# Optimization experiments

Measured on AMD Instinct MI355X. Metric: run time of the kernel, lower is better.

Reference implementation:

```python
import jax, jax.numpy as jnp
import numpy as np

NENTITY = 200000
NRELATION = 500
HIDDEN = 256
GAMMA = 12.0
EPS = 2.0
EMB_RANGE = (GAMMA + EPS) / HIDDEN


def setup_inputs() -> dict:
    key = jax.random.key(0)
    ks = jax.random.split(key, 8)
    B, NEG = 256, 1024
    head = jax.random.randint(ks[0], (B, 1), 0, NENTITY)
    tail = jax.random.randint(ks[1], (B, NEG), 0, NENTITY)
    relation = jax.random.randint(ks[2], (B,), 0, NRELATION)
    entity_emb = jax.random.uniform(ks[3], (NENTITY, HIDDEN), jnp.float32, -EMB_RANGE, EMB_RANGE)
    relation_emb = jax.random.uniform(ks[4], (NRELATION, 2 * HIDDEN), jnp.float32, -EMB_RANGE, EMB_RANGE)
    lim = 1.0 / np.sqrt(2 * HIDDEN)
    W_fc = jax.random.uniform(ks[5], (HIDDEN, 2 * HIDDEN), jnp.float32, -lim, lim)
    b_fc = jax.random.uniform(ks[6], (HIDDEN,), jnp.float32, -lim, lim)
    return {"head": head, "tail": tail, "relation": relation,
            "entity_emb": entity_emb, "relation_emb": relation_emb,
            "W_fc": W_fc, "b_fc": b_fc}


def _l2_normalize(x):
    # F.normalize(x, p=2, dim=-1): x / max(||x||_2, 1e-12)
    n = jnp.sqrt(jnp.sum(x * x, axis=-1, keepdims=True))
    return x / jnp.maximum(n, 1e-12)


def reference(head, tail, relation, entity_emb, relation_emb, W_fc, b_fc):
    # gather embeddings
    h = entity_emb[head]                      # [B, 1,   d]
    t = entity_emb[tail]                      # [B, NEG, d]
    r = relation_emb[relation][:, None, :]    # [B, 1, 2d]
    re_head, re_tail = jnp.split(r, 2, axis=-1)   # each [B, 1, d]
    # broadcast relation halves to match head/tail sample counts, then concat
    re_h = jnp.broadcast_to(re_head, h.shape)
    re_t = jnp.broadcast_to(re_tail, t.shape)
    h_cat = jnp.concatenate([h, re_h], axis=-1)   # [B, 1,   2d]
    t_cat = jnp.concatenate([t, re_t], axis=-1)   # [B, NEG, 2d]
    # shared small FC (torch Linear: x @ W^T + b)
    h_fc = jnp.einsum('bnk,dk->bnd', h_cat, W_fc) + b_fc
    t_fc = jnp.einsum('bnk,dk->bnd', t_cat, W_fc) + b_fc
    h_n = _l2_normalize(h_fc)
    t_n = _l2_normalize(t_fc)
    diff = h_n - t_n                              # [B, NEG, d]
    score = GAMMA - jnp.sum(jnp.abs(diff), axis=2)  # [B, NEG]
    return score
```

## Files before the change

kernel.cpp:

```cpp
#include <hip/hip_runtime.h>
#include <math.h>

#define NENTITY 200000
#define HIDDEN 256
#define NEG 1024
#define NBATCH 256
#define GAMMA_F 12.0f
#define BM 32
#define NTILES 8
#define NBLK 1024
#define NT_P 8
#define CHUNK 128

typedef short v8s __attribute__((ext_vector_type(8)));
typedef float v4f __attribute__((ext_vector_type(4)));
typedef unsigned int u32;

#define LDS_BARRIER() asm volatile("s_waitcnt lgkmcnt(0)\n\ts_barrier" ::: "memory")

__device__ __forceinline__ short f2bf(float x) {
    u32 u = __float_as_uint(x);
    u = (u + 0x7fffu + ((u >> 16) & 1u)) >> 16;
    return (short)u;
}

__device__ __forceinline__ u32 rhu(float f) { return __float_as_uint(f) + 0x8000u; }
__device__ __forceinline__ v8s pack8(const float4& x0, const float4& x1) {
    int4 fr;
    fr.x = __builtin_amdgcn_perm(rhu(x0.y), rhu(x0.x), 0x07060302u);
    fr.y = __builtin_amdgcn_perm(rhu(x0.w), rhu(x0.z), 0x07060302u);
    fr.z = __builtin_amdgcn_perm(rhu(x1.y), rhu(x1.x), 0x07060302u);
    fr.w = __builtin_amdgcn_perm(rhu(x1.w), rhu(x1.z), 0x07060302u);
    return __builtin_bit_cast(v8s, fr);
}
__device__ __forceinline__ uint2 pack4(const v4f& a) {
    uint2 pk;
    pk.x = __builtin_amdgcn_perm(rhu(a[1]), rhu(a[0]), 0x07060302u);
    pk.y = __builtin_amdgcn_perm(rhu(a[3]), rhu(a[2]), 0x07060302u);
    return pk;
}

__global__ __launch_bounds__(256) void prep_kernel(
    const int* __restrict__ head, const int* __restrict__ relation,
    const float* __restrict__ entity_emb, const float* __restrict__ relation_emb,
    const float* __restrict__ W_fc, const float* __restrict__ b_fc,
    short* __restrict__ W1bf, float* __restrict__ h_n, float* __restrict__ rel_part)
{
    const int b = blockIdx.x;
    const int t = threadIdx.x;

    W1bf[b * HIDDEN + t] = f2bf(W_fc[(size_t)b * 2 * HIDDEN + t]);

    __shared__ float xh[2 * HIDDEN];
    __shared__ float xt[HIDDEN];
    __shared__ float red[256];

    const int hidx = head[b];
    const int r = relation[b];
    xh[t]          = entity_emb[(size_t)hidx * HIDDEN + t];
    xh[HIDDEN + t] = relation_emb[(size_t)r * 2 * HIDDEN + t];
    xt[t]          = relation_emb[(size_t)r * 2 * HIDDEN + HIDDEN + t];
    __syncthreads();

    const float4* wrow = reinterpret_cast<const float4*>(W_fc + (size_t)t * 2 * HIDDEN);
    float hf = b_fc[t];
    float rp = b_fc[t];
    #pragma unroll 4
    for (int kk = 0; kk < HIDDEN / 4; ++kk) {
        float4 w = wrow[kk];
        hf += xh[4*kk+0]*w.x + xh[4*kk+1]*w.y + xh[4*kk+2]*w.z + xh[4*kk+3]*w.w;
    }
    #pragma unroll 4
    for (int kk = 0; kk < HIDDEN / 4; ++kk) {
        float4 w = wrow[HIDDEN/4 + kk];
        hf += xh[HIDDEN+4*kk+0]*w.x + xh[HIDDEN+4*kk+1]*w.y + xh[HIDDEN+4*kk+2]*w.z + xh[HIDDEN+4*kk+3]*w.w;
        rp += xt[4*kk+0]*w.x + xt[4*kk+1]*w.y + xt[4*kk+2]*w.z + xt[4*kk+3]*w.w;
    }
    rel_part[b * HIDDEN + t] = rp;

    red[t] = hf * hf;
    __syncthreads();
    for (int s = 128; s > 0; s >>= 1) {
        if (t < s) red[t] += red[t + s];
        __syncthreads();
    }
    const float norm = sqrtf(red[0]);
    h_n[b * HIDDEN + t] = hf / fmaxf(norm, 1e-12f);
}

__global__ __launch_bounds__(512, 4) void proj_kernel(
    const float* __restrict__ entity_emb, const short* __restrict__ W1bf,
    short* __restrict__ P)
{
    __shared__ __align__(16) short Abf[2][BM * HIDDEN];

    const int t = threadIdx.x;
    const int w = t >> 6;
    const int l = t & 63;
    const int c = t & 15;
    const int g = (t >> 4) & 3;
    const int E0 = blockIdx.x * (NT_P * BM);

    v8s Wf[2][8];
    #pragma unroll
    for (int f2 = 0; f2 < 2; ++f2) {
        const short* bsrc = W1bf + (size_t)(w * 32 + f2 * 16 + c) * HIDDEN + g * 8;
        #pragma unroll
        for (int kt = 0; kt < 8; ++kt)
            Wf[f2][kt] = *reinterpret_cast<const v8s*>(bsrc + kt * 32);
    }
    #pragma unroll
    for (int f2 = 0; f2 < 2; ++f2)
        #pragma unroll
        for (int kt = 0; kt < 8; ++kt)
            asm volatile("" : "+v"(Wf[f2][kt]));

    v4f st[4];
    auto issue = [&](int j) {
        #pragma unroll
        for (int i = 0; i < 4; ++i) {
            int row = E0 + j * BM + w * 4 + i;
            row = row < NENTITY ? row : NENTITY - 1;
            st[i] = *reinterpret_cast<const v4f*>(
                entity_emb + (size_t)row * HIDDEN + (l << 2));
        }
        __builtin_amdgcn_sched_barrier(0);
    };
    auto commit = [&](int buf) {
        char* base = reinterpret_cast<char*>(&Abf[buf][0]);
        #pragma unroll
        for (int i = 0; i < 4; ++i) {
            const int r = w * 4 + i;
            uint2 pk = pack4(st[i]);
            *reinterpret_cast<uint2*>(base + r * 512
                + (((l >> 1) ^ (r & 7)) << 4) + ((l & 1) << 3)) = pk;
        }
    };

    issue(0);
    commit(0);
    LDS_BARRIER();

    #pragma unroll 1
    for (int j = 0; j < NT_P; ++j) {
        const int cur = j & 1;
        if (j + 1 < NT_P) issue(j + 1);

        v4f acc[2][2];
        #pragma unroll
        for (int et = 0; et < 2; ++et)
            #pragma unroll
            for (int f2 = 0; f2 < 2; ++f2)
                acc[et][f2] = v4f{0.f, 0.f, 0.f, 0.f};

        const char* base = reinterpret_cast<const char*>(&Abf[cur][0]);
        const int swz = c & 7;

        #pragma unroll
        for (int kt = 0; kt < 8; ++kt) {
            const int u = ((kt * 4 + g) ^ swz) << 4;
            v8s e0 = *reinterpret_cast<const v8s*>(base + (c)      * 512 + u);
            v8s e1 = *reinterpret_cast<const v8s*>(base + (16 + c) * 512 + u);
            #pragma unroll
            for (int f2 = 0; f2 < 2; ++f2) {
                acc[0][f2] = __builtin_amdgcn_mfma_f32_16x16x32_bf16(Wf[f2][kt], e0, acc[0][f2], 0, 0, 0);
                acc[1][f2] = __builtin_amdgcn_mfma_f32_16x16x32_bf16(Wf[f2][kt], e1, acc[1][f2], 0, 0, 0);
            }
        }

        if (j + 1 < NT_P) commit(cur ^ 1);

        #pragma unroll
        for (int et = 0; et < 2; ++et) {
            const int e = E0 + j * BM + et * 16 + c;
            if (e < NENTITY) {
                short* dst = P + (size_t)e * HIDDEN + w * 32 + g * 4;
                #pragma unroll
                for (int f2 = 0; f2 < 2; ++f2)
                    *reinterpret_cast<uint2*>(dst + f2 * 16) = pack4(acc[et][f2]);
            }
        }

        LDS_BARRIER();
    }
}

__global__ __launch_bounds__(256) void score2_kernel(
    const int* __restrict__ tail, const short* __restrict__ P,
    const float* __restrict__ h_n, const float* __restrict__ rel_part,
    float* __restrict__ out)
{
    const int t = threadIdx.x;
    const int w = t >> 6;
    const int l = t & 63;
    const int b = blockIdx.x >> 3;
    const int chunk = blockIdx.x & 7;
    const int base = b * NEG + chunk * CHUNK;

    __shared__ int tl[CHUNK];
    if (t < CHUNK) tl[t] = tail[base + t];

    const float4 hh = *reinterpret_cast<const float4*>(h_n + b * HIDDEN + 4 * l);
    const float4 rp = *reinterpret_cast<const float4*>(rel_part + b * HIDDEN + 4 * l);
    __syncthreads();

    uint2 st2[8];
    #pragma unroll
    for (int i = 0; i < 8; ++i)
        st2[i] = *(reinterpret_cast<const uint2*>(P + (size_t)tl[w * 32 + i] * HIDDEN) + l);

    #pragma unroll
    for (int p = 0; p < 32; ++p) {
        uint2 v = st2[p & 7];
        if (p + 8 < 32)
            st2[p & 7] = *(reinterpret_cast<const uint2*>(
                P + (size_t)tl[w * 32 + p + 8] * HIDDEN) + l);

        float t0 = __uint_as_float(v.x << 16)          + rp.x;
        float t1 = __uint_as_float(v.x & 0xffff0000u)  + rp.y;
        float t2 = __uint_as_float(v.y << 16)          + rp.z;
        float t3 = __uint_as_float(v.y & 0xffff0000u)  + rp.w;

        float ssq = t0 * t0 + t1 * t1 + t2 * t2 + t3 * t3;
        #pragma unroll
        for (int mask = 1; mask < 64; mask <<= 1) ssq += __shfl_xor(ssq, mask);
        const float rn = 1.f / fmaxf(sqrtf(ssq), 1e-12f);

        float l1 = fabsf(hh.x - t0 * rn) + fabsf(hh.y - t1 * rn)
                 + fabsf(hh.z - t2 * rn) + fabsf(hh.w - t3 * rn);
        #pragma unroll
        for (int mask = 1; mask < 64; mask <<= 1) l1 += __shfl_xor(l1, mask);

        if (l == 0) out[base + w * 32 + p] = GAMMA_F - l1;
    }
}

__global__ __launch_bounds__(256, 2) void score_kernel(
    const int* __restrict__ tail, const float* __restrict__ entity_emb,
    const short* __restrict__ W1bf, const float* __restrict__ h_n,
    const float* __restrict__ rel_part, float* __restrict__ out)
{
    __shared__ __align__(16) float Asf[2][BM * HIDDEN];
    __shared__ int tails[NTILES * BM];
    __shared__ float ssq_lds[4][BM];
    __shared__ float l1_lds[4][BM];

    const int t = threadIdx.x;
    const int w = t >> 6;
    const int l = t & 63;
    const int c = t & 15;
    const int g = (t >> 4) & 3;
    const int b = blockIdx.x >> 2;

    tails[t] = tail[blockIdx.x * (NTILES * BM) + t];

    float rlv[4], hnv[4];
    #pragma unroll
    for (int ntl = 0; ntl < 4; ++ntl) {
        const int n = 64 * w + ntl * 16 + c;
        rlv[ntl] = rel_part[b * HIDDEN + n];
        hnv[ntl] = h_n[b * HIDDEN + n];
    }

    v8s Bf[4][8];
    #pragma unroll
    for (int ntl = 0; ntl < 4; ++ntl) {
        const short* bsrc = W1bf + (size_t)(64 * w + ntl * 16 + c) * HIDDEN + g * 8;
        #pragma unroll
        for (int kt = 0; kt < 8; ++kt)
            Bf[ntl][kt] = *reinterpret_cast<const v8s*>(bsrc + kt * 32);
    }

    __syncthreads();

    v4f st[8];
    auto issue = [&](int j) {
        #pragma unroll
        for (int i = 0; i < 8; ++i) {
            const int r = w * 8 + i;
            const float* src = entity_emb + (size_t)tails[j * BM + r] * HIDDEN + (l << 2);
            st[i] = *reinterpret_cast<const v4f*>(src);
        }
        __builtin_amdgcn_sched_barrier(0);
    };
    auto commit = [&](int buf) {
        #pragma unroll
        for (int i = 0; i < 8; ++i) {
            const int r = w * 8 + i;
            *reinterpret_cast<v4f*>(&Asf[buf][r * HIDDEN + ((l ^ (r & 7)) << 2)]) = st[i];
        }
    };

    issue(0);
    commit(0);
    LDS_BARRIER();

    #pragma unroll 1
    for (int j = 0; j < NTILES; ++j) {
        const int cur = j & 1;
        if (j + 1 < NTILES) issue(j + 1);

        v4f acc[2][4];
        #pragma unroll
        for (int mt = 0; mt < 2; ++mt)
            #pragma unroll
            for (int ntl = 0; ntl < 4; ++ntl)
                acc[mt][ntl] = v4f{0.f, 0.f, 0.f, 0.f};

        const float* a0base = &Asf[cur][c * HIDDEN];
        const float* a1base = &Asf[cur][(16 + c) * HIDDEN];
        const int swz = c & 7;

        #pragma unroll
        for (int kt = 0; kt < 8; ++kt) {
            const int u0 = kt * 8 + g * 2;
            float4 x0 = *reinterpret_cast<const float4*>(a0base + (((u0    ) ^ swz) << 2));
            float4 x1 = *reinterpret_cast<const float4*>(a0base + (((u0 + 1) ^ swz) << 2));
            float4 y0 = *reinterpret_cast<const float4*>(a1base + (((u0    ) ^ swz) << 2));
            float4 y1 = *reinterpret_cast<const float4*>(a1base + (((u0 + 1) ^ swz) << 2));
            v8s a0 = pack8(x0, x1);
            v8s a1 = pack8(y0, y1);
            #pragma unroll
            for (int ntl = 0; ntl < 4; ++ntl) {
                acc[0][ntl] = __builtin_amdgcn_mfma_f32_16x16x32_bf16(a0, Bf[ntl][kt], acc[0][ntl], 0, 0, 0);
                acc[1][ntl] = __builtin_amdgcn_mfma_f32_16x16x32_bf16(a1, Bf[ntl][kt], acc[1][ntl], 0, 0, 0);
            }
        }

        #pragma unroll
        for (int mt = 0; mt < 2; ++mt) {
            float ssq[4] = {0.f, 0.f, 0.f, 0.f};
            #pragma unroll
            for (int ntl = 0; ntl < 4; ++ntl) {
                #pragma unroll
                for (int r = 0; r < 4; ++r) {
                    float tf = acc[mt][ntl][r] + rlv[ntl];
                    acc[mt][ntl][r] = tf;
                    ssq[r] += tf * tf;
                }
            }
            #pragma unroll
            for (int mask = 1; mask < 16; mask <<= 1) {
                #pragma unroll
                for (int r = 0; r < 4; ++r) ssq[r] += __shfl_xor(ssq[r], mask);
            }
            if (c == 0) {
                #pragma unroll
                for (int r = 0; r < 4; ++r) ssq_lds[w][mt * 16 + g * 4 + r] = ssq[r];
            }
        }
        LDS_BARRIER();

        #pragma unroll
        for (int mt = 0; mt < 2; ++mt) {
            float rn[4], s1[4] = {0.f, 0.f, 0.f, 0.f};
            #pragma unroll
            for (int r = 0; r < 4; ++r) {
                const int m = mt * 16 + g * 4 + r;
                float tot = ssq_lds[0][m] + ssq_lds[1][m] + ssq_lds[2][m] + ssq_lds[3][m];
                rn[r] = 1.f / fmaxf(sqrtf(tot), 1e-12f);
            }
            #pragma unroll
            for (int ntl = 0; ntl < 4; ++ntl) {
                #pragma unroll
                for (int r = 0; r < 4; ++r)
                    s1[r] += fabsf(hnv[ntl] - acc[mt][ntl][r] * rn[r]);
            }
            #pragma unroll
            for (int mask = 1; mask < 16; mask <<= 1) {
                #pragma unroll
                for (int r = 0; r < 4; ++r) s1[r] += __shfl_xor(s1[r], mask);
            }
            if (c == 0) {
                #pragma unroll
                for (int r = 0; r < 4; ++r) l1_lds[w][mt * 16 + g * 4 + r] = s1[r];
            }
        }

        if (j + 1 < NTILES) commit(cur ^ 1);
        LDS_BARRIER();

        if (t < BM) {
            out[blockIdx.x * (NTILES * BM) + j * BM + t] = GAMMA_F -
                (l1_lds[0][t] + l1_lds[1][t] + l1_lds[2][t] + l1_lds[3][t]);
        }
    }
}

extern "C" void kernel_launch(void* const* d_in, const int* in_sizes, int n_in,
                              void* d_out, int out_size, void* d_ws, size_t ws_size,
                              hipStream_t stream)
{
    const int*   head         = (const int*)d_in[0];
    const int*   tail         = (const int*)d_in[1];
    const int*   relation     = (const int*)d_in[2];
    const float* entity_emb   = (const float*)d_in[3];
    const float* relation_emb = (const float*)d_in[4];
    const float* W_fc         = (const float*)d_in[5];
    const float* b_fc         = (const float*)d_in[6];
    float* out = (float*)d_out;

    short* W1bf     = (short*)d_ws;
    float* h_n      = (float*)((char*)d_ws + 131072);
    float* rel_part = (float*)((char*)d_ws + 131072 + 262144);

    prep_kernel<<<NBATCH, 256, 0, stream>>>(head, relation, entity_emb, relation_emb,
                                            W_fc, b_fc, W1bf, h_n, rel_part);

    const size_t P_OFF   = 1ull << 20;
    const size_t P_BYTES = (size_t)NENTITY * HIDDEN * sizeof(short);
    if (ws_size >= P_OFF + P_BYTES) {
        short* P = (short*)((char*)d_ws + P_OFF);
        const int grid = (NENTITY + NT_P * BM - 1) / (NT_P * BM);
        proj_kernel<<<grid, 512, 0, stream>>>(entity_emb, W1bf, P);
        score2_kernel<<<NBATCH * 8, 256, 0, stream>>>(tail, P, h_n, rel_part, out);
    } else {
        score_kernel<<<NBLK, 256, 0, stream>>>(tail, entity_emb, W1bf,
                                               h_n, rel_part, out);
    }
}
```

Before: 396.8 us.

## Load entity rows straight into MFMA operand registers in persistent projection kernel

```diff
diff --git a/kernel.cpp b/kernel.cpp
--- a/kernel.cpp
+++ b/kernel.cpp
@@ -9,7 +9,8 @@
 #define BM 32
 #define NTILES 8
 #define NBLK 1024
-#define NT_P 8
+#define GRPS (NENTITY / 16)
+#define PROJ_GRID 512
 #define CHUNK 128
 
 typedef short v8s __attribute__((ext_vector_type(8)));
@@ -25,12 +26,12 @@
 }
 
 __device__ __forceinline__ u32 rhu(float f) { return __float_as_uint(f) + 0x8000u; }
-__device__ __forceinline__ v8s pack8(const float4& x0, const float4& x1) {
+__device__ __forceinline__ v8s pack8(const v4f& x0, const v4f& x1) {
     int4 fr;
-    fr.x = __builtin_amdgcn_perm(rhu(x0.y), rhu(x0.x), 0x07060302u);
-    fr.y = __builtin_amdgcn_perm(rhu(x0.w), rhu(x0.z), 0x07060302u);
-    fr.z = __builtin_amdgcn_perm(rhu(x1.y), rhu(x1.x), 0x07060302u);
-    fr.w = __builtin_amdgcn_perm(rhu(x1.w), rhu(x1.z), 0x07060302u);
+    fr.x = __builtin_amdgcn_perm(rhu(x0[1]), rhu(x0[0]), 0x07060302u);
+    fr.y = __builtin_amdgcn_perm(rhu(x0[3]), rhu(x0[2]), 0x07060302u);
+    fr.z = __builtin_amdgcn_perm(rhu(x1[1]), rhu(x1[0]), 0x07060302u);
+    fr.w = __builtin_amdgcn_perm(rhu(x1[3]), rhu(x1[2]), 0x07060302u);
     return __builtin_bit_cast(v8s, fr);
 }
 __device__ __forceinline__ uint2 pack4(const v4f& a) {
@@ -88,18 +89,14 @@
     h_n[b * HIDDEN + t] = hf / fmaxf(norm, 1e-12f);
 }
 
-__global__ __launch_bounds__(512, 4) void proj_kernel(
+__global__ __launch_bounds__(512, 2) void proj_kernel(
     const float* __restrict__ entity_emb, const short* __restrict__ W1bf,
     short* __restrict__ P)
 {
-    __shared__ __align__(16) short Abf[2][BM * HIDDEN];
-
     const int t = threadIdx.x;
     const int w = t >> 6;
-    const int l = t & 63;
     const int c = t & 15;
     const int g = (t >> 4) & 3;
-    const int E0 = blockIdx.x * (NT_P * BM);
 
     v8s Wf[2][8];
     #pragma unroll
@@ -115,73 +112,44 @@
         for (int kt = 0; kt < 8; ++kt)
             asm volatile("" : "+v"(Wf[f2][kt]));
 
-    v4f st[4];
-    auto issue = [&](int j) {
-        #pragma unroll
-        for (int i = 0; i < 4; ++i) {
-            int row = E0 + j * BM + w * 4 + i;
-            row = row < NENTITY ? row : NENTITY - 1;
-            st[i] = *reinterpret_cast<const v4f*>(
-                entity_emb + (size_t)row * HIDDEN + (l << 2));
-        }
+    v4f st[16];
+    auto issue = [&](int grp) {
+        const float* rowp = entity_emb + (size_t)(grp * 16 + c) * HIDDEN + g * 8;
+        #pragma unroll
+        for (int kt = 0; kt < 8; ++kt) {
+            st[2 * kt]     = *reinterpret_cast<const v4f*>(rowp + kt * 32);
+            st[2 * kt + 1] = *reinterpret_cast<const v4f*>(rowp + kt * 32 + 4);
+        }
+    };
+
+    int grp = blockIdx.x;
+    issue(grp);
+
+    #pragma unroll 1
+    for (; grp < GRPS; grp += PROJ_GRID) {
+        int ng = grp + PROJ_GRID;
+        if (ng >= GRPS) ng = grp;
+
+        v8s bf[8];
+        #pragma unroll
+        for (int kt = 0; kt < 8; ++kt)
+            bf[kt] = pack8(st[2 * kt], st[2 * kt + 1]);
+
+        issue(ng);
         __builtin_amdgcn_sched_barrier(0);
-    };
-    auto commit = [&](int buf) {
-        char* base = reinterpret_cast<char*>(&Abf[buf][0]);
-        #pragma unroll
-        for (int i = 0; i < 4; ++i) {
-            const int r = w * 4 + i;
-            uint2 pk = pack4(st[i]);
-            *reinterpret_cast<uint2*>(base + r * 512
-                + (((l >> 1) ^ (r & 7)) << 4) + ((l & 1) << 3)) = pk;
-        }
-    };
-
-    issue(0);
-    commit(0);
-    LDS_BARRIER();
-
-    #pragma unroll 1
-    for (int j = 0; j < NT_P; ++j) {
-        const int cur = j & 1;
-        if (j + 1 < NT_P) issue(j + 1);
-
-        v4f acc[2][2];
-        #pragma unroll
-        for (int et = 0; et < 2; ++et)
-            #pragma unroll
-            for (int f2 = 0; f2 < 2; ++f2)
-                acc[et][f2] = v4f{0.f, 0.f, 0.f, 0.f};
-
-        const char* base = reinterpret_cast<const char*>(&Abf[cur][0]);
-        const int swz = c & 7;
-
+
+        v4f acc[2];
+        acc[0] = v4f{0.f, 0.f, 0.f, 0.f};
+        acc[1] = v4f{0.f, 0.f, 0.f, 0.f};
         #pragma unroll
         for (int kt = 0; kt < 8; ++kt) {
-            const int u = ((kt * 4 + g) ^ swz) << 4;
-            v8s e0 = *reinterpret_cast<const v8s*>(base + (c)      * 512 + u);
-            v8s e1 = *reinterpret_cast<const v8s*>(base + (16 + c) * 512 + u);
-            #pragma unroll
-            for (int f2 = 0; f2 < 2; ++f2) {
-                acc[0][f2] = __builtin_amdgcn_mfma_f32_16x16x32_bf16(Wf[f2][kt], e0, acc[0][f2], 0, 0, 0);
-                acc[1][f2] = __builtin_amdgcn_mfma_f32_16x16x32_bf16(Wf[f2][kt], e1, acc[1][f2], 0, 0, 0);
-            }
-        }
-
-        if (j + 1 < NT_P) commit(cur ^ 1);
-
-        #pragma unroll
-        for (int et = 0; et < 2; ++et) {
-            const int e = E0 + j * BM + et * 16 + c;
-            if (e < NENTITY) {
-                short* dst = P + (size_t)e * HIDDEN + w * 32 + g * 4;
-                #pragma unroll
-                for (int f2 = 0; f2 < 2; ++f2)
-                    *reinterpret_cast<uint2*>(dst + f2 * 16) = pack4(acc[et][f2]);
-            }
-        }
-
-        LDS_BARRIER();
+            acc[0] = __builtin_amdgcn_mfma_f32_16x16x32_bf16(Wf[0][kt], bf[kt], acc[0], 0, 0, 0);
+            acc[1] = __builtin_amdgcn_mfma_f32_16x16x32_bf16(Wf[1][kt], bf[kt], acc[1], 0, 0, 0);
+        }
+
+        short* dst = P + (size_t)(grp * 16 + c) * HIDDEN + w * 32 + g * 4;
+        *reinterpret_cast<uint2*>(dst)      = pack4(acc[0]);
+        *reinterpret_cast<uint2*>(dst + 16) = pack4(acc[1]);
     }
 }
 
@@ -314,10 +282,10 @@
         #pragma unroll
         for (int kt = 0; kt < 8; ++kt) {
             const int u0 = kt * 8 + g * 2;
-            float4 x0 = *reinterpret_cast<const float4*>(a0base + (((u0    ) ^ swz) << 2));
-            float4 x1 = *reinterpret_cast<const float4*>(a0base + (((u0 + 1) ^ swz) << 2));
-            float4 y0 = *reinterpret_cast<const float4*>(a1base + (((u0    ) ^ swz) << 2));
-            float4 y1 = *reinterpret_cast<const float4*>(a1base + (((u0 + 1) ^ swz) << 2));
+            v4f x0 = *reinterpret_cast<const v4f*>(a0base + (((u0    ) ^ swz) << 2));
+            v4f x1 = *reinterpret_cast<const v4f*>(a0base + (((u0 + 1) ^ swz) << 2));
+            v4f y0 = *reinterpret_cast<const v4f*>(a1base + (((u0    ) ^ swz) << 2));
+            v4f y1 = *reinterpret_cast<const v4f*>(a1base + (((u0 + 1) ^ swz) << 2));
             v8s a0 = pack8(x0, x1);
             v8s a1 = pack8(y0, y1);
             #pragma unroll
@@ -411,8 +379,7 @@
     const size_t P_BYTES = (size_t)NENTITY * HIDDEN * sizeof(short);
     if (ws_size >= P_OFF + P_BYTES) {
         short* P = (short*)((char*)d_ws + P_OFF);
-        const int grid = (NENTITY + NT_P * BM - 1) / (NT_P * BM);
-        proj_kernel<<<grid, 512, 0, stream>>>(entity_emb, W1bf, P);
+        proj_kernel<<<PROJ_GRID, 512, 0, stream>>>(entity_emb, W1bf, P);
         score2_kernel<<<NBATCH * 8, 256, 0, stream>>>(tail, P, h_n, rel_part, out);
     } else {
         score_kernel<<<NBLK, 256, 0, stream>>>(tail, entity_emb, W1bf,
```

Result: slower. 499.1 us (+25.8%).
